# Optimization experiments

Measured on AMD Instinct MI355X. Metric: run time of the kernel, lower is better.

Reference implementation:

```python
import jax, jax.numpy as jnp
import numpy as np
from jax import lax

B, L, H2, T = 128, 1024, 1024, 9  # batch, seq_len, 2*hidden_dim (multichannel), tag_num


def setup_inputs() -> dict:
    key = jax.random.key(0)
    k1, k2, k3, k4, k5, k6 = jax.random.split(key, 6)
    encoder_output = jax.random.normal(k1, (B, L, H2), jnp.float32)
    lengths = jax.random.randint(k2, (B,), L // 2, L + 1)
    mask = jnp.arange(L)[None, :] < lengths[:, None]  # [B, L] bool, mask[:,0] all True
    W = jax.random.normal(k3, (T, H2), jnp.float32) * 0.02  # hidden2label weight
    b = jnp.zeros((T,), jnp.float32)                         # hidden2label bias
    start_transitions = jax.random.uniform(k4, (T,), jnp.float32, -0.1, 0.1)
    end_transitions = jax.random.uniform(k5, (T,), jnp.float32, -0.1, 0.1)
    transitions = jax.random.uniform(k6, (T, T), jnp.float32, -0.1, 0.1)
    return {"encoder_output": encoder_output, "mask": mask, "W": W, "b": b,
            "start_transitions": start_transitions, "end_transitions": end_transitions,
            "transitions": transitions}


def _viterbi(emissions, mask, start_transitions, end_transitions, transitions):
    # emissions [B,L,T], mask [B,L] bool. Mirrors torchcrf CRF._viterbi_decode.
    Bn, Ln, Tn = emissions.shape
    score0 = start_transitions[None, :] + emissions[:, 0]  # [B,T]
    iden = jnp.arange(Tn, dtype=jnp.int32)[None, :]

    def step(score, inp):
        emit, m = inp  # emit [B,T], m [B]
        # next_score[b, i, j] = score[b,i] + transitions[i,j] + emit[b,j]
        nxt = score[:, :, None] + transitions[None] + emit[:, None, :]  # [B,T,T]
        best = jnp.max(nxt, axis=1)                      # [B,T]
        idx = jnp.argmax(nxt, axis=1).astype(jnp.int32)  # [B,T] best prev tag
        new_score = jnp.where(m[:, None], best, score)
        idx = jnp.where(m[:, None], idx, iden)           # frozen steps: carry same tag
        return new_score, idx

    emits = jnp.transpose(emissions[:, 1:], (1, 0, 2))  # [L-1,B,T]
    ms = mask[:, 1:].T                                   # [L-1,B]
    final, hist = lax.scan(step, score0, (emits, ms))
    final = final + end_transitions[None, :]
    best_score = jnp.max(final, axis=-1)                     # [B]
    last_tag = jnp.argmax(final, axis=-1).astype(jnp.int32)  # [B]

    def back(tag, idx):  # tag [B] is tag at time j+1; idx [B,T] history at step j
        prev = jnp.take_along_axis(idx, tag[:, None], axis=1)[:, 0]
        return prev, tag

    tag0, tags_rest = lax.scan(back, last_tag, hist, reverse=True)  # tags_rest[j] = tag_{j+1}
    tags = jnp.concatenate([tag0[None], tags_rest], axis=0)  # [L,B]
    tags = jnp.transpose(tags, (1, 0))                        # [B,L]
    tags = jnp.where(mask, tags, 0)                           # zero out padding
    return tags, best_score


def reference(encoder_output, mask, W, b, start_transitions, end_transitions, transitions):
    # hidden2label: Linear(2H -> T)
    emissions = jnp.einsum('blh,th->blt', encoder_output, W) + b[None, None, :]
    tags, best_score = _viterbi(emissions, mask, start_transitions, end_transitions, transitions)
    return tags, best_score
```

## Files before the change

### kernel.cpp

```cpp
#include <hip/hip_runtime.h>
#include <stdint.h>

#define Bn 128
#define Ln 1024
#define H2n 1024
#define Tn 9
#define Cn 32
#define Sn 32
#define GPW 7
#define WPB 5
#define EP 12
#define HP 16
#define NEG (-1e30f)


__device__ __forceinline__ int mask_mode(const void* m) {
    const uint8_t* p = (const uint8_t*)m;
    return (p[1] == 1) ? 0 : ((p[4] == 1) ? 1 : 2);
}
__device__ __forceinline__ bool mask_get(const void* m, int mode, int idx) {
    if (mode == 0) return ((const uint8_t*)m)[idx] != 0;
    if (mode == 1) return ((const int*)m)[idx] != 0;
    return ((const long long*)m)[idx] != 0;
}

__global__ __launch_bounds__(64) void k_len(const void* __restrict__ mask,
                                            int* __restrict__ lenw) {
    const int b = blockIdx.x;
    const int lane = threadIdx.x;
    const int mode = mask_mode(mask);
    int cnt = 0;
    for (int k = 0; k < Ln / 64; ++k)
        cnt += mask_get(mask, mode, b * Ln + lane + k * 64) ? 1 : 0;
#pragma unroll
    for (int off = 32; off > 0; off >>= 1) cnt += __shfl_xor(cnt, off, 64);
    if (lane == 0) lenw[b] = cnt;
}

__global__ __launch_bounds__(256) void k_emis(const float* __restrict__ enc,
                                              const float* __restrict__ W,
                                              const float* __restrict__ bias,
                                              float* __restrict__ emis) {
    __shared__ float Wl[Tn * H2n];
    __shared__ float bl[Tn];
    const int tid = threadIdx.x;
    for (int i = tid; i < Tn * H2n; i += 256) Wl[i] = W[i];
    if (tid < Tn) bl[tid] = bias[tid];
    __syncthreads();

    const int lane = tid & 63;
    const int wave = tid >> 6;
    const int wid  = blockIdx.x * 4 + wave;
    const int row0 = wid * 32;

    for (int rr = 0; rr < 32; ++rr) {
        const int row = row0 + rr;
        const float4* rp = (const float4*)(enc + (size_t)row * H2n);
        float acc[Tn];
#pragma unroll
        for (int t = 0; t < Tn; ++t) acc[t] = 0.f;
#pragma unroll
        for (int j = 0; j < 4; ++j) {
            const float4 ev = rp[lane + j * 64];
#pragma unroll
            for (int t = 0; t < Tn; ++t) {
                const float4 wv = ((const float4*)(Wl + t * H2n))[lane + j * 64];
                acc[t] += ev.x * wv.x + ev.y * wv.y + ev.z * wv.z + ev.w * wv.w;
            }
        }
#pragma unroll
        for (int t = 0; t < Tn; ++t) {
#pragma unroll
            for (int off = 32; off > 0; off >>= 1)
                acc[t] += __shfl_xor(acc[t], off, 64);
        }
        if (lane == 0) {
            float* op = emis + (size_t)row * EP;
            *((float4*)op)       = make_float4(acc[0] + bl[0], acc[1] + bl[1],
                                               acc[2] + bl[2], acc[3] + bl[3]);
            *((float4*)(op + 4)) = make_float4(acc[4] + bl[4], acc[5] + bl[5],
                                               acc[6] + bl[6], acc[7] + bl[7]);
            *((float4*)(op + 8)) = make_float4(acc[8] + bl[8], 0.f, 0.f, 0.f);
        }
    }
}

__global__ __launch_bounds__(64) void k_chunkmat(const float* __restrict__ emis,
                                                 const float* __restrict__ trans,
                                                 const int* __restrict__ lenw,
                                                 float* __restrict__ Mws) {
    const int b = blockIdx.x / WPB;
    const int w = blockIdx.x % WPB;
    const int lane = threadIdx.x;
    const int cs = lane / 9, i = lane % 9;
    const int c = w * GPW + cs;
    const bool act = (lane < 63) && (c < Cn);
    const int cc = act ? c : 0;
    const int len = lenw[b];

    float tr[81];
#pragma unroll
    for (int k = 0; k < 81; ++k) tr[k] = trans[k];

    float m[9];
#pragma unroll
    for (int k = 0; k < 9; ++k) m[k] = (k == i) ? 0.f : NEG;

    const float* erow = emis + (size_t)b * Ln * EP;
    const int l0 = 1 + cc * Sn;
#pragma unroll
    for (int t = 0; t < Sn; ++t) {
        const int l = l0 + t;
        const int le = (l < Ln) ? l : (Ln - 1);
        const float4 ea = *((const float4*)(erow + le * EP));
        const float4 eb4 = *((const float4*)(erow + le * EP + 4));
        const float e8v = erow[le * EP + 8];
        const float e[9] = {ea.x, ea.y, ea.z, ea.w, eb4.x, eb4.y, eb4.z, eb4.w, e8v};
        const bool ds = act && (l < len);
        float nm[9];
#pragma unroll
        for (int j = 0; j < 9; ++j) {
            float v = m[0] + tr[j];
#pragma unroll
            for (int k = 1; k < 9; ++k) v = fmaxf(v, m[k] + tr[k * 9 + j]);
            nm[j] = v + e[j];
        }
#pragma unroll
        for (int j = 0; j < 9; ++j) m[j] = ds ? nm[j] : m[j];
    }
    if (act) {
        float* Mr = Mws + ((size_t)(b * Cn + c) * 9 + i) * EP;
        *((float4*)Mr)       = make_float4(m[0], m[1], m[2], m[3]);
        *((float4*)(Mr + 4)) = make_float4(m[4], m[5], m[6], m[7]);
        *((float4*)(Mr + 8)) = make_float4(m[8], 0.f, 0.f, 0.f);
    }
}

__global__ __launch_bounds__(64) void k_stitch_scores(const float* __restrict__ emis,
                                                      const float* __restrict__ Mws,
                                                      const float* __restrict__ startT,
                                                      const float* __restrict__ endT,
                                                      float* __restrict__ sb,
                                                      float* __restrict__ score_out,
                                                      int* __restrict__ ltag) {
    const int b = blockIdx.x;
    const int lane = threadIdx.x;
    const int j = (lane < Tn) ? lane : 0;
    float s = startT[j] + emis[(size_t)b * Ln * EP + j];
    for (int c = 0; c < Cn; ++c) {
        if (lane < Tn) sb[(size_t)(b * Cn + c) * EP + j] = s;
        float sf[9];
#pragma unroll
        for (int k = 0; k < 9; ++k) sf[k] = __shfl(s, k, 64);
        const float* Mc = Mws + (size_t)(b * Cn + c) * 9 * EP;
        float v = sf[0] + Mc[j];
#pragma unroll
        for (int k = 1; k < 9; ++k) v = fmaxf(v, sf[k] + Mc[k * EP + j]);
        s = v;
    }
    s += endT[j];
    float sf[9];
#pragma unroll
    for (int k = 0; k < 9; ++k) sf[k] = __shfl(s, k, 64);
    if (lane == 0) {
        float best = sf[0]; int bi = 0;
#pragma unroll
        for (int k = 1; k < 9; ++k) if (sf[k] > best) { best = sf[k]; bi = k; }
        score_out[b] = best;
        ltag[b] = bi;
    }
}

__global__ __launch_bounds__(64) void k_replay(const float* __restrict__ emis,
                                               const float* __restrict__ trans,
                                               const int* __restrict__ lenw,
                                               const float* __restrict__ sb,
                                               uint8_t* __restrict__ hist,
                                               uint8_t* __restrict__ comp) {
    const int b = blockIdx.x / WPB;
    const int w = blockIdx.x % WPB;
    const int lane = threadIdx.x;
    const int cs = lane / 9, j = lane % 9;
    const int c = w * GPW + cs;
    const bool act = (lane < 63) && (c < Cn);
    const int cc = act ? c : 0;
    const int base = cs * 9;
    const int len = lenw[b];

    float tcol[9];
#pragma unroll
    for (int i = 0; i < 9; ++i) tcol[i] = trans[i * 9 + j];

    float s = sb[(size_t)(b * Cn + cc) * EP + j];
    int cmp = j;
    const float* erow = emis + (size_t)b * Ln * EP;
    uint8_t* hb = hist + (size_t)b * Ln * HP;
    const int l0 = 1 + cc * Sn;

    for (int t = 0; t < Sn; ++t) {
        const int l = l0 + t;
        const int le = (l < Ln) ? l : (Ln - 1);
        float sf[9];
#pragma unroll
        for (int i = 0; i < 9; ++i) sf[i] = __shfl(s, base + i, 64);
        float best = sf[0] + tcol[0]; int idx = 0;
#pragma unroll
        for (int i = 1; i < 9; ++i) {
            const float v = sf[i] + tcol[i];
            if (v > best) { best = v; idx = i; }
        }
        const bool msk = act && (l < len);
        const float em = erow[le * EP + j];
        s = msk ? best + em : s;
        idx = msk ? idx : j;
        if (act && l < Ln) hb[l * HP + j] = (uint8_t)idx;
        cmp = __shfl(cmp, base + idx, 64);
    }
    if (act) comp[(size_t)(b * Cn + c) * HP + j] = (uint8_t)cmp;
}

__global__ __launch_bounds__(64) void k_stitch_tags(const uint8_t* __restrict__ comp,
                                                    const int* __restrict__ ltag,
                                                    uint8_t* __restrict__ bt,
                                                    float* __restrict__ tags) {
    const int b = blockIdx.x * 64 + threadIdx.x;
    if (b >= Bn) return;
    int t = ltag[b];
    for (int c = Cn - 1; c >= 0; --c) {
        bt[b * Cn + c] = (uint8_t)t;
        t = comp[(size_t)(b * Cn + c) * HP + t];
    }
    tags[(size_t)b * Ln] = (float)t;
}

__global__ __launch_bounds__(64) void k_writetags(const uint8_t* __restrict__ hist,
                                                  const uint8_t* __restrict__ bt,
                                                  const int* __restrict__ lenw,
                                                  float* __restrict__ tags) {
    const int g = blockIdx.x * 64 + threadIdx.x;
    const int b = g >> 5, c = g & 31;
    const int len = lenw[b];
    const uint8_t* hb = hist + (size_t)b * Ln * HP;
    int t = bt[b * Cn + c];
    const int lo = 1 + c * Sn;
    const int hi = (lo + Sn < Ln) ? lo + Sn : Ln;
    for (int l = hi - 1; l >= lo; --l) {
        tags[(size_t)b * Ln + l] = (l < len) ? (float)t : 0.f;
        t = hb[l * HP + t];
    }
}

extern "C" void kernel_launch(void* const* d_in, const int* in_sizes, int n_in,
                              void* d_out, int out_size, void* d_ws, size_t ws_size,
                              hipStream_t stream) {
    const float* enc    = (const float*)d_in[0];
    const void*  mask   = d_in[1];
    const float* W      = (const float*)d_in[2];
    const float* bias   = (const float*)d_in[3];
    const float* startT = (const float*)d_in[4];
    const float* endT   = (const float*)d_in[5];
    const float* trans  = (const float*)d_in[6];

    float* out_tags  = (float*)d_out;
    float* out_score = out_tags + (size_t)Bn * Ln;

    char* ws = (char*)d_ws;
    float*   emis = (float*)(ws);
    float*   Mws  = (float*)(ws + 6291456);
    float*   sb   = (float*)(ws + 8060928);
    uint8_t* hist = (uint8_t*)(ws + 8257536);
    uint8_t* comp = (uint8_t*)(ws + 10354688);
    int*     lenw = (int*)(ws + 10420224);
    int*     ltag = (int*)(ws + 10420736);
    uint8_t* bt   = (uint8_t*)(ws + 10421248);

    k_len<<<Bn, 64, 0, stream>>>(mask, lenw);
    k_emis<<<1024, 256, 0, stream>>>(enc, W, bias, emis);
    k_chunkmat<<<Bn * WPB, 64, 0, stream>>>(emis, trans, lenw, Mws);
    k_stitch_scores<<<Bn, 64, 0, stream>>>(emis, Mws, startT, endT, sb, out_score, ltag);
    k_replay<<<Bn * WPB, 64, 0, stream>>>(emis, trans, lenw, sb, hist, comp);
    k_stitch_tags<<<(Bn + 63) / 64, 64, 0, stream>>>(comp, ltag, bt, out_tags);
    k_writetags<<<64, 64, 0, stream>>>(hist, bt, lenw, out_tags);
}
```

Baseline: 770.2 us.

## Fuse all Viterbi stages into one per-batch kernel with shared-memory intermediates

Replaces six separate kernels (length count, chunk matrices, score stitching, replay, tag stitching, tag writeback) with a single kernel of one 320-thread block per batch row. Intermediates such as chunk matrices, boundary scores, history and compressed backpointers live in LDS instead of global workspace, and the steps are separated by __syncthreads. This removes launch gaps and global round-trips but uses only 128 blocks. The serial stitch phases now run inside the block while the other waves sit idle.

Measured after the change: 732.6 us. 4.9% less time.

```diff
diff --git a/kernel.cpp b/kernel.cpp
--- a/kernel.cpp
+++ b/kernel.cpp
@@ -8,7 +8,6 @@
 #define Cn 32
 #define Sn 32
 #define GPW 7
-#define WPB 5
 #define EP 12
 #define HP 16
 #define NEG (-1e30f)
@@ -22,19 +21,6 @@
     if (mode == 0) return ((const uint8_t*)m)[idx] != 0;
     if (mode == 1) return ((const int*)m)[idx] != 0;
     return ((const long long*)m)[idx] != 0;
-}
-
-__global__ __launch_bounds__(64) void k_len(const void* __restrict__ mask,
-                                            int* __restrict__ lenw) {
-    const int b = blockIdx.x;
-    const int lane = threadIdx.x;
-    const int mode = mask_mode(mask);
-    int cnt = 0;
-    for (int k = 0; k < Ln / 64; ++k)
-        cnt += mask_get(mask, mode, b * Ln + lane + k * 64) ? 1 : 0;
-#pragma unroll
-    for (int off = 32; off > 0; off >>= 1) cnt += __shfl_xor(cnt, off, 64);
-    if (lane == 0) lenw[b] = cnt;
 }
 
 __global__ __launch_bounds__(256) void k_emis(const float* __restrict__ enc,
@@ -85,169 +71,164 @@
     }
 }
 
-__global__ __launch_bounds__(64) void k_chunkmat(const float* __restrict__ emis,
-                                                 const float* __restrict__ trans,
-                                                 const int* __restrict__ lenw,
-                                                 float* __restrict__ Mws) {
-    const int b = blockIdx.x / WPB;
-    const int w = blockIdx.x % WPB;
-    const int lane = threadIdx.x;
-    const int cs = lane / 9, i = lane % 9;
-    const int c = w * GPW + cs;
+__global__ __launch_bounds__(320) void k_viterbi_all(const float* __restrict__ emis,
+                                                     const void* __restrict__ maskraw,
+                                                     const float* __restrict__ startT,
+                                                     const float* __restrict__ endT,
+                                                     const float* __restrict__ trans,
+                                                     float* __restrict__ tags,
+                                                     float* __restrict__ score_out) {
+    __shared__ float   Ml[Cn * 9 * EP];
+    __shared__ float   sbl[Cn * EP];
+    __shared__ uint8_t hl[Ln * HP];
+    __shared__ uint8_t cl[Cn * HP];
+    __shared__ uint8_t btl[Cn];
+    __shared__ uint8_t tagrow[Ln];
+    __shared__ int lenl, ltagl;
+
+    const int b    = blockIdx.x;
+    const int tid  = threadIdx.x;
+    const int wave = tid >> 6;
+    const int lane = tid & 63;
+
+    if (wave == 0) {
+        const int mode = mask_mode(maskraw);
+        int cnt = 0;
+        for (int k = 0; k < Ln / 64; ++k)
+            cnt += mask_get(maskraw, mode, b * Ln + lane + k * 64) ? 1 : 0;
+#pragma unroll
+        for (int off = 32; off > 0; off >>= 1) cnt += __shfl_xor(cnt, off, 64);
+        if (lane == 0) lenl = cnt;
+    }
+    __syncthreads();
+    const int len = lenl;
+
+    const float* erow = emis + (size_t)b * Ln * EP;
+    const int cs = lane / 9;
+    const int ii = lane % 9;
+    const int c  = wave * GPW + cs;
     const bool act = (lane < 63) && (c < Cn);
     const int cc = act ? c : 0;
-    const int len = lenw[b];
-
-    float tr[81];
-#pragma unroll
-    for (int k = 0; k < 81; ++k) tr[k] = trans[k];
-
-    float m[9];
-#pragma unroll
-    for (int k = 0; k < 9; ++k) m[k] = (k == i) ? 0.f : NEG;
-
-    const float* erow = emis + (size_t)b * Ln * EP;
     const int l0 = 1 + cc * Sn;
-#pragma unroll
-    for (int t = 0; t < Sn; ++t) {
-        const int l = l0 + t;
-        const int le = (l < Ln) ? l : (Ln - 1);
-        const float4 ea = *((const float4*)(erow + le * EP));
-        const float4 eb4 = *((const float4*)(erow + le * EP + 4));
-        const float e8v = erow[le * EP + 8];
-        const float e[9] = {ea.x, ea.y, ea.z, ea.w, eb4.x, eb4.y, eb4.z, eb4.w, e8v};
-        const bool ds = act && (l < len);
-        float nm[9];
-#pragma unroll
-        for (int j = 0; j < 9; ++j) {
-            float v = m[0] + tr[j];
-#pragma unroll
-            for (int k = 1; k < 9; ++k) v = fmaxf(v, m[k] + tr[k * 9 + j]);
-            nm[j] = v + e[j];
-        }
-#pragma unroll
-        for (int j = 0; j < 9; ++j) m[j] = ds ? nm[j] : m[j];
-    }
-    if (act) {
-        float* Mr = Mws + ((size_t)(b * Cn + c) * 9 + i) * EP;
-        *((float4*)Mr)       = make_float4(m[0], m[1], m[2], m[3]);
-        *((float4*)(Mr + 4)) = make_float4(m[4], m[5], m[6], m[7]);
-        *((float4*)(Mr + 8)) = make_float4(m[8], 0.f, 0.f, 0.f);
-    }
-}
-
-__global__ __launch_bounds__(64) void k_stitch_scores(const float* __restrict__ emis,
-                                                      const float* __restrict__ Mws,
-                                                      const float* __restrict__ startT,
-                                                      const float* __restrict__ endT,
-                                                      float* __restrict__ sb,
-                                                      float* __restrict__ score_out,
-                                                      int* __restrict__ ltag) {
-    const int b = blockIdx.x;
-    const int lane = threadIdx.x;
-    const int j = (lane < Tn) ? lane : 0;
-    float s = startT[j] + emis[(size_t)b * Ln * EP + j];
-    for (int c = 0; c < Cn; ++c) {
-        if (lane < Tn) sb[(size_t)(b * Cn + c) * EP + j] = s;
+
+    {
+        float tr[81];
+#pragma unroll
+        for (int k = 0; k < 81; ++k) tr[k] = trans[k];
+        float m[9];
+#pragma unroll
+        for (int k = 0; k < 9; ++k) m[k] = (k == ii) ? 0.f : NEG;
+#pragma unroll
+        for (int t = 0; t < Sn; ++t) {
+            const int l = l0 + t;
+            const int le = (l < Ln) ? l : (Ln - 1);
+            const float4 ea  = *((const float4*)(erow + le * EP));
+            const float4 eb4 = *((const float4*)(erow + le * EP + 4));
+            const float  e8v = erow[le * EP + 8];
+            const float e[9] = {ea.x, ea.y, ea.z, ea.w, eb4.x, eb4.y, eb4.z, eb4.w, e8v};
+            const bool ds = act && (l < len);
+            float nm[9];
+#pragma unroll
+            for (int j = 0; j < 9; ++j) {
+                float v = m[0] + tr[j];
+#pragma unroll
+                for (int k = 1; k < 9; ++k) v = fmaxf(v, m[k] + tr[k * 9 + j]);
+                nm[j] = v + e[j];
+            }
+#pragma unroll
+            for (int j = 0; j < 9; ++j) m[j] = ds ? nm[j] : m[j];
+        }
+        if (act) {
+            float* Mr = Ml + (size_t)(c * 9 + ii) * EP;
+            *((float4*)Mr)       = make_float4(m[0], m[1], m[2], m[3]);
+            *((float4*)(Mr + 4)) = make_float4(m[4], m[5], m[6], m[7]);
+            *((float4*)(Mr + 8)) = make_float4(m[8], 0.f, 0.f, 0.f);
+        }
+    }
+    __syncthreads();
+
+    if (wave == 0) {
+        const int j = (lane < Tn) ? lane : 0;
+        float s = startT[j] + erow[j];
+        for (int c2 = 0; c2 < Cn; ++c2) {
+            if (lane < Tn) sbl[c2 * EP + j] = s;
+            float sf[9];
+#pragma unroll
+            for (int k = 0; k < 9; ++k) sf[k] = __shfl(s, k, 64);
+            const float* Mc = Ml + (size_t)c2 * 9 * EP;
+            float v = sf[0] + Mc[j];
+#pragma unroll
+            for (int k = 1; k < 9; ++k) v = fmaxf(v, sf[k] + Mc[k * EP + j]);
+            s = v;
+        }
+        s += endT[j];
         float sf[9];
 #pragma unroll
         for (int k = 0; k < 9; ++k) sf[k] = __shfl(s, k, 64);
-        const float* Mc = Mws + (size_t)(b * Cn + c) * 9 * EP;
-        float v = sf[0] + Mc[j];
-#pragma unroll
-        for (int k = 1; k < 9; ++k) v = fmaxf(v, sf[k] + Mc[k * EP + j]);
-        s = v;
-    }
-    s += endT[j];
-    float sf[9];
-#pragma unroll
-    for (int k = 0; k < 9; ++k) sf[k] = __shfl(s, k, 64);
-    if (lane == 0) {
-        float best = sf[0]; int bi = 0;
-#pragma unroll
-        for (int k = 1; k < 9; ++k) if (sf[k] > best) { best = sf[k]; bi = k; }
-        score_out[b] = best;
-        ltag[b] = bi;
-    }
-}
-
-__global__ __launch_bounds__(64) void k_replay(const float* __restrict__ emis,
-                                               const float* __restrict__ trans,
-                                               const int* __restrict__ lenw,
-                                               const float* __restrict__ sb,
-                                               uint8_t* __restrict__ hist,
-                                               uint8_t* __restrict__ comp) {
-    const int b = blockIdx.x / WPB;
-    const int w = blockIdx.x % WPB;
-    const int lane = threadIdx.x;
-    const int cs = lane / 9, j = lane % 9;
-    const int c = w * GPW + cs;
-    const bool act = (lane < 63) && (c < Cn);
-    const int cc = act ? c : 0;
-    const int base = cs * 9;
-    const int len = lenw[b];
-
-    float tcol[9];
-#pragma unroll
-    for (int i = 0; i < 9; ++i) tcol[i] = trans[i * 9 + j];
-
-    float s = sb[(size_t)(b * Cn + cc) * EP + j];
-    int cmp = j;
-    const float* erow = emis + (size_t)b * Ln * EP;
-    uint8_t* hb = hist + (size_t)b * Ln * HP;
-    const int l0 = 1 + cc * Sn;
-
-    for (int t = 0; t < Sn; ++t) {
-        const int l = l0 + t;
-        const int le = (l < Ln) ? l : (Ln - 1);
-        float sf[9];
-#pragma unroll
-        for (int i = 0; i < 9; ++i) sf[i] = __shfl(s, base + i, 64);
-        float best = sf[0] + tcol[0]; int idx = 0;
-#pragma unroll
-        for (int i = 1; i < 9; ++i) {
-            const float v = sf[i] + tcol[i];
-            if (v > best) { best = v; idx = i; }
-        }
-        const bool msk = act && (l < len);
-        const float em = erow[le * EP + j];
-        s = msk ? best + em : s;
-        idx = msk ? idx : j;
-        if (act && l < Ln) hb[l * HP + j] = (uint8_t)idx;
-        cmp = __shfl(cmp, base + idx, 64);
-    }
-    if (act) comp[(size_t)(b * Cn + c) * HP + j] = (uint8_t)cmp;
-}
-
-__global__ __launch_bounds__(64) void k_stitch_tags(const uint8_t* __restrict__ comp,
-                                                    const int* __restrict__ ltag,
-                                                    uint8_t* __restrict__ bt,
-                                                    float* __restrict__ tags) {
-    const int b = blockIdx.x * 64 + threadIdx.x;
-    if (b >= Bn) return;
-    int t = ltag[b];
-    for (int c = Cn - 1; c >= 0; --c) {
-        bt[b * Cn + c] = (uint8_t)t;
-        t = comp[(size_t)(b * Cn + c) * HP + t];
-    }
-    tags[(size_t)b * Ln] = (float)t;
-}
-
-__global__ __launch_bounds__(64) void k_writetags(const uint8_t* __restrict__ hist,
-                                                  const uint8_t* __restrict__ bt,
-                                                  const int* __restrict__ lenw,
-                                                  float* __restrict__ tags) {
-    const int g = blockIdx.x * 64 + threadIdx.x;
-    const int b = g >> 5, c = g & 31;
-    const int len = lenw[b];
-    const uint8_t* hb = hist + (size_t)b * Ln * HP;
-    int t = bt[b * Cn + c];
-    const int lo = 1 + c * Sn;
-    const int hi = (lo + Sn < Ln) ? lo + Sn : Ln;
-    for (int l = hi - 1; l >= lo; --l) {
-        tags[(size_t)b * Ln + l] = (l < len) ? (float)t : 0.f;
-        t = hb[l * HP + t];
-    }
+        if (lane == 0) {
+            float best = sf[0]; int bi = 0;
+#pragma unroll
+            for (int k = 1; k < 9; ++k) if (sf[k] > best) { best = sf[k]; bi = k; }
+            score_out[b] = best;
+            ltagl = bi;
+        }
+    }
+    __syncthreads();
+
+    {
+        const int j = ii;
+        const int base = cs * 9;
+        float tcol[9];
+#pragma unroll
+        for (int i = 0; i < 9; ++i) tcol[i] = trans[i * 9 + j];
+        float s = sbl[cc * EP + j];
+        int cmp = j;
+        for (int t = 0; t < Sn; ++t) {
+            const int l = l0 + t;
+            const int le = (l < Ln) ? l : (Ln - 1);
+            float sf[9];
+#pragma unroll
+            for (int i = 0; i < 9; ++i) sf[i] = __shfl(s, base + i, 64);
+            float best = sf[0] + tcol[0]; int idx = 0;
+#pragma unroll
+            for (int i = 1; i < 9; ++i) {
+                const float v = sf[i] + tcol[i];
+                if (v > best) { best = v; idx = i; }
+            }
+            const bool msk = act && (l < len);
+            const float em = erow[le * EP + j];
+            s = msk ? best + em : s;
+            idx = msk ? idx : j;
+            if (act && l < Ln) hl[l * HP + j] = (uint8_t)idx;
+            cmp = __shfl(cmp, base + idx, 64);
+        }
+        if (act) cl[c * HP + j] = (uint8_t)cmp;
+    }
+    __syncthreads();
+
+    if (tid == 0) {
+        int t = ltagl;
+        for (int c2 = Cn - 1; c2 >= 0; --c2) {
+            btl[c2] = (uint8_t)t;
+            t = cl[c2 * HP + t];
+        }
+        tagrow[0] = (uint8_t)t;
+    }
+    __syncthreads();
+
+    if (tid < Cn) {
+        int t = btl[tid];
+        const int lo = 1 + tid * Sn;
+        const int hi = (lo + Sn < Ln) ? lo + Sn : Ln;
+        for (int l = hi - 1; l >= lo; --l) {
+            tagrow[l] = (l < len) ? (uint8_t)t : 0;
+            t = hl[l * HP + t];
+        }
+    }
+    __syncthreads();
+
+    for (int l = tid; l < Ln; l += 320)
+        tags[(size_t)b * Ln + l] = (float)tagrow[l];
 }
 
 extern "C" void kernel_launch(void* const* d_in, const int* in_sizes, int n_in,
@@ -264,21 +245,9 @@
     float* out_tags  = (float*)d_out;
     float* out_score = out_tags + (size_t)Bn * Ln;
 
-    char* ws = (char*)d_ws;
-    float*   emis = (float*)(ws);
-    float*   Mws  = (float*)(ws + 6291456);
-    float*   sb   = (float*)(ws + 8060928);
-    uint8_t* hist = (uint8_t*)(ws + 8257536);
-    uint8_t* comp = (uint8_t*)(ws + 10354688);
-    int*     lenw = (int*)(ws + 10420224);
-    int*     ltag = (int*)(ws + 10420736);
-    uint8_t* bt   = (uint8_t*)(ws + 10421248);
-
-    k_len<<<Bn, 64, 0, stream>>>(mask, lenw);
+    float* emis = (float*)d_ws;
+
     k_emis<<<1024, 256, 0, stream>>>(enc, W, bias, emis);
-    k_chunkmat<<<Bn * WPB, 64, 0, stream>>>(emis, trans, lenw, Mws);
-    k_stitch_scores<<<Bn, 64, 0, stream>>>(emis, Mws, startT, endT, sb, out_score, ltag);
-    k_replay<<<Bn * WPB, 64, 0, stream>>>(emis, trans, lenw, sb, hist, comp);
-    k_stitch_tags<<<(Bn + 63) / 64, 64, 0, stream>>>(comp, ltag, bt, out_tags);
-    k_writetags<<<64, 64, 0, stream>>>(hist, bt, lenw, out_tags);
-}
+    k_viterbi_all<<<Bn, 320, 0, stream>>>(emis, mask, startT, endT, trans,
+                                          out_tags, out_score);
+}
```
